# Performance work log

Hardware: AMD Instinct MI355X
Metric: run time of the kernel (lower is better)

Reference implementation:

```python
import jax, jax.numpy as jnp
import numpy as np

N = 50000        # nodes
E = 800000       # edges
H = 128          # hidden_channels
NH = 4           # num_heads
HD = H // NH     # head_dim
EPS = 1e-5       # LayerNorm eps (torch default)


def setup_inputs() -> dict:
    key = jax.random.key(0)
    ks = jax.random.split(key, 16)
    s = 0.02
    return {
        "x": jax.random.normal(ks[0], (N, H), dtype=jnp.float32),
        "edge_index": jax.random.randint(ks[1], (2, E), 0, N, dtype=jnp.int64),
        "Wq": jax.random.normal(ks[2], (H, H), dtype=jnp.float32) * s,
        "bq": jnp.zeros((H,), jnp.float32),
        "Wk": jax.random.normal(ks[3], (H, H), dtype=jnp.float32) * s,
        "bk": jnp.zeros((H,), jnp.float32),
        "Wv": jax.random.normal(ks[4], (H, H), dtype=jnp.float32) * s,
        "bv": jnp.zeros((H,), jnp.float32),
        "W1": jax.random.normal(ks[5], (2 * H, H), dtype=jnp.float32) * s,
        "b1": jnp.zeros((H,), jnp.float32),
        "ln_g": jnp.ones((H,), jnp.float32),
        "ln_b": jnp.zeros((H,), jnp.float32),
        "W2": jax.random.normal(ks[6], (H, H), dtype=jnp.float32) * s,
        "b2": jnp.zeros((H,), jnp.float32),
    }


def reference(x, edge_index, Wq, bq, Wk, bk, Wv, bv, W1, b1, ln_g, ln_b, W2, b2):
    n = x.shape[0]
    row, col = edge_index[0], edge_index[1]
    # dense projections, split heads: [N, NH, HD]
    Q = (x @ Wq + bq).reshape(n, NH, HD)
    K = (x @ Wk + bk).reshape(n, NH, HD)
    V = (x @ Wv + bv).reshape(n, NH, HD)
    # edge-wise gather + per-head dot product: [E, NH]
    scores = (Q[row] * K[col]).sum(-1) / jnp.sqrt(jnp.float32(HD))
    # segment softmax over edges grouped by destination node (row)
    m = jax.ops.segment_max(scores, row, num_segments=n)        # [N, NH]
    m = jnp.where(jnp.isfinite(m), m, 0.0)                      # empty segments -> 0
    e = jnp.exp(scores - m[row])                                # [E, NH]
    denom = jax.ops.segment_sum(e, row, num_segments=n)         # [N, NH]
    w = e / denom[row]                                          # [E, NH]
    # weighted scatter-add aggregation: [N, H]
    msg = (w[..., None] * V[col]).reshape(-1, NH * HD)          # [E, H]
    agg = jax.ops.segment_sum(msg, row, num_segments=n)         # [N, H]
    # MLP: Linear -> ReLU -> LayerNorm -> Linear, plus residual
    h = jax.nn.relu(jnp.concatenate([x, agg], axis=-1) @ W1 + b1)
    mu = h.mean(-1, keepdims=True)
    var = ((h - mu) ** 2).mean(-1, keepdims=True)
    h = (h - mu) / jnp.sqrt(var + EPS) * ln_g + ln_b
    return h @ W2 + b2 + x
```

## Files before the change

### kernel.cpp

```cpp
#include <hip/hip_runtime.h>
#include <hip/hip_bf16.h>

#define NN 50000
#define HH 128
#define NHEAD 4
#define HD 32
#define EE 800000
#define LN_EPS 1e-5f
#define ROWS_PAD 50048
#define SCAN_NB 98

typedef __bf16 bf16x8 __attribute__((ext_vector_type(8)));
typedef short  s16x8  __attribute__((ext_vector_type(8)));
typedef float  f32x4  __attribute__((ext_vector_type(4)));

__device__ __forceinline__ f32x4 mfma_bf16(s16x8 a, s16x8 b, f32x4 c) {
    return __builtin_amdgcn_mfma_f32_16x16x32_bf16((bf16x8)a, (bf16x8)b, c, 0, 0, 0);
}

__device__ __forceinline__ unsigned short f2bf(float f) {
    union { float f; unsigned int u; } v; v.f = f;
    unsigned int u = v.u + 0x7FFFu + ((v.u >> 16) & 1u);
    return (unsigned short)(u >> 16);
}
__device__ __forceinline__ float bf2f(unsigned short h) {
    union { unsigned int u; float f; } v; v.u = ((unsigned int)h) << 16;
    return v.f;
}
__device__ __forceinline__ float bflo(unsigned int w) { return __uint_as_float(w << 16); }
__device__ __forceinline__ float bfhi(unsigned int w) { return __uint_as_float(w & 0xffff0000u); }

__global__ void detect_idx_kernel(const unsigned int* __restrict__ buf, int* __restrict__ flag) {
    if (blockIdx.x == 0 && threadIdx.x == 0) {
        int is64 = 1;
        for (int i = 0; i < 64; ++i) {
            if (buf[2 * i + 1] != 0u) { is64 = 0; break; }
        }
        *flag = is64;
    }
}

__global__ void hist_kernel(const void* __restrict__ ei, const int* __restrict__ flag,
                            int* __restrict__ deg, int* __restrict__ rank) {
    int i = (blockIdx.x * blockDim.x + threadIdx.x) * 2;
    if (i >= EE) return;
    int r0, r1;
    if (*flag) {
        longlong2 rv = *(const longlong2*)((const long long*)ei + i);
        r0 = (int)rv.x; r1 = (int)rv.y;
    } else {
        int2 rv = *(const int2*)((const int*)ei + i);
        r0 = rv.x; r1 = rv.y;
    }
    int ra = atomicAdd(&deg[r0], 1);
    int rb = atomicAdd(&deg[r1], 1);
    *(int2*)(rank + i) = make_int2(ra, rb);
}

__global__ __launch_bounds__(512) void scan_a_kernel(const int* __restrict__ deg,
                                                     int* __restrict__ bsum) {
    __shared__ int red[8];
    const int t = threadIdx.x;
    const int gid = blockIdx.x * 512 + t;
    int v = (gid < NN) ? deg[gid] : 0;
    #pragma unroll
    for (int o = 1; o < 64; o <<= 1) v += __shfl_xor(v, o);
    if ((t & 63) == 0) red[t >> 6] = v;
    __syncthreads();
    if (t == 0) {
        int s = 0;
        #pragma unroll
        for (int k = 0; k < 8; ++k) s += red[k];
        bsum[blockIdx.x] = s;
    }
}

__global__ __launch_bounds__(512) void scan_c_kernel(const int* __restrict__ deg,
                                                     const int* __restrict__ bsum,
                                                     int* __restrict__ rstart) {
    __shared__ int wsum[8];
    __shared__ int blockoff;
    const int t = threadIdx.x;
    const int gid = blockIdx.x * 512 + t;
    const int lane = t & 63, w = t >> 6;
    if (t < 64) {
        int s = 0;
        for (int k = t; k < blockIdx.x; k += 64) s += bsum[k];
        #pragma unroll
        for (int o = 1; o < 64; o <<= 1) s += __shfl_xor(s, o);
        if (t == 0) blockoff = s;
    }
    int v = (gid < NN) ? deg[gid] : 0;
    int incl = v;
    #pragma unroll
    for (int o = 1; o < 64; o <<= 1) {
        int u = __shfl_up(incl, o);
        if (lane >= o) incl += u;
    }
    if (lane == 63) wsum[w] = incl;
    __syncthreads();
    int woff = 0;
    for (int k = 0; k < w; ++k) woff += wsum[k];
    int excl = blockoff + woff + incl - v;
    if (gid < NN) rstart[gid] = excl;
    if (gid == 0) rstart[NN] = EE;
}

__global__ void scatter_kernel(const void* __restrict__ ei, const int* __restrict__ flag,
                               const int* __restrict__ rank, const int* __restrict__ rstart,
                               int* __restrict__ colS) {
    int i = (blockIdx.x * blockDim.x + threadIdx.x) * 2;
    if (i >= EE) return;
    int r0, r1, c0, c1;
    if (*flag) {
        longlong2 rv = *(const longlong2*)((const long long*)ei + i);
        longlong2 cv = *(const longlong2*)((const long long*)ei + EE + i);
        r0 = (int)rv.x; r1 = (int)rv.y;
        c0 = (int)cv.x; c1 = (int)cv.y;
    } else {
        int2 rv = *(const int2*)((const int*)ei + i);
        int2 cv = *(const int2*)((const int*)ei + EE + i);
        r0 = rv.x; r1 = rv.y;
        c0 = cv.x; c1 = cv.y;
    }
    int2 rk = *(const int2*)(rank + i);
    colS[rstart[r0] + rk.x] = c0;
    colS[rstart[r1] + rk.y] = c1;
}

__global__ void pack_w_kernel(const float* __restrict__ Wq, const float* __restrict__ Wk,
                              const float* __restrict__ Wv, const float* __restrict__ W1,
                              const float* __restrict__ W2, unsigned short* __restrict__ wf) {
    int i = blockIdx.x * blockDim.x + threadIdx.x;
    if (i >= 98304) return;
    float val;
    if (i < 49152) {
        int j = i & 7, lane = (i >> 3) & 63, kk = (i >> 9) & 3, nt = i >> 11;
        int k = kk * 32 + (lane >> 4) * 8 + j;
        int n = nt * 16 + (lane & 15);
        const float* W = (n < 128) ? Wq : ((n < 256) ? Wk : Wv);
        val = W[k * HH + (n & 127)];
    } else if (i < 81920) {
        int local = i - 49152;
        int j = local & 7, lane = (local >> 3) & 63, kk = (local >> 9) & 7, nt = local >> 12;
        int k = kk * 32 + (lane >> 4) * 8 + j;
        int n = nt * 16 + (lane & 15);
        val = W1[k * HH + n];
    } else {
        int local = i - 81920;
        int j = local & 7, lane = (local >> 3) & 63, kk = (local >> 9) & 3, nt = local >> 11;
        int k = kk * 32 + (lane >> 4) * 8 + j;
        int n = nt * 16 + (lane & 15);
        val = W2[k * HH + n];
    }
    wf[i] = f2bf(val);
}

__global__ __launch_bounds__(256) void qkvx_kernel(
        const float* __restrict__ x, const unsigned short* __restrict__ wf,
        const float* __restrict__ bq, const float* __restrict__ bk, const float* __restrict__ bv,
        unsigned short* __restrict__ xa,
        unsigned short* __restrict__ Qb, unsigned short* __restrict__ Kb,
        unsigned short* __restrict__ Vb) {
    const int wave = threadIdx.x >> 6, lane = threadIdx.x & 63;
    const int row0 = blockIdx.x * 64 + wave * 16;
    const int arow = row0 + (lane & 15);
    const int kbase = (lane >> 4) * 8;

    s16x8 a[4];
    if (arow < NN) {
        const float* xp = x + (size_t)arow * HH + kbase;
        #pragma unroll
        for (int kk = 0; kk < 4; ++kk) {
            float4 f0 = *(const float4*)(xp + kk * 32);
            float4 f1 = *(const float4*)(xp + kk * 32 + 4);
            s16x8 av;
            av[0] = (short)f2bf(f0.x); av[1] = (short)f2bf(f0.y);
            av[2] = (short)f2bf(f0.z); av[3] = (short)f2bf(f0.w);
            av[4] = (short)f2bf(f1.x); av[5] = (short)f2bf(f1.y);
            av[6] = (short)f2bf(f1.z); av[7] = (short)f2bf(f1.w);
            a[kk] = av;
            *(s16x8*)(xa + (size_t)arow * 256 + kbase + kk * 32) = av;
        }
    } else {
        #pragma unroll
        for (int kk = 0; kk < 4; ++kk) a[kk] = (s16x8)0;
    }

    f32x4 acc[24];
    #pragma unroll
    for (int nt = 0; nt < 24; ++nt) acc[nt] = (f32x4){0.f, 0.f, 0.f, 0.f};

    const s16x8* wfv = (const s16x8*)wf;
    #pragma unroll
    for (int nt = 0; nt < 24; ++nt) {
        #pragma unroll
        for (int kk = 0; kk < 4; ++kk) {
            s16x8 b = wfv[(nt * 4 + kk) * 64 + lane];
            acc[nt] = mfma_bf16(a[kk], b, acc[nt]);
        }
    }

    const int colb = lane & 15;
    const int rbase = row0 + (lane >> 4) * 4;
    #pragma unroll
    for (int nt = 0; nt < 24; ++nt) {
        const int mtx = nt >> 3;
        const int nc = (nt & 7) * 16 + colb;
        const float* bias_p = (mtx == 0) ? bq : ((mtx == 1) ? bk : bv);
        unsigned short* O = (mtx == 0) ? Qb : ((mtx == 1) ? Kb : Vb);
        float bias = bias_p[nc];
        #pragma unroll
        for (int r = 0; r < 4; ++r)
            O[(size_t)(rbase + r) * 128 + nc] = f2bf(acc[nt][r] + bias);
    }
}

__global__ __launch_bounds__(256) void attn_kernel(
        const unsigned short* __restrict__ Qb, const unsigned short* __restrict__ Kb,
        const unsigned short* __restrict__ Vb, const int* __restrict__ rstart,
        const int* __restrict__ colS, unsigned short* __restrict__ xa) {
    const int wave = threadIdx.x >> 6;
    const int lane = threadIdx.x & 63;
    const int h = lane & 3;
    const int le = lane >> 2;
    const int half = lane >> 5;
    const int sl = lane & 31;
    const int g2 = sl >> 3;
    const int ibase = blockIdx.x * 16 + wave * 4;

    for (int j = 0; j < 4; ++j) {
        const int i = ibase + j;
        const int e0 = rstart[i], e1 = rstart[i + 1];
        const int deg = e1 - e0;

        float qf[32];
        {
            const uint4* qp = (const uint4*)(Qb + (size_t)i * 128 + h * 32);
            #pragma unroll
            for (int cch = 0; cch < 4; ++cch) {
                uint4 qv = qp[cch];
                unsigned int w_[4] = {qv.x, qv.y, qv.z, qv.w};
                #pragma unroll
                for (int dd = 0; dd < 4; ++dd) {
                    qf[cch * 8 + dd * 2]     = bflo(w_[dd]);
                    qf[cch * 8 + dd * 2 + 1] = bfhi(w_[dd]);
                }
            }
        }

        float m = -INFINITY, l = 0.f;
        float acc0 = 0.f, acc1 = 0.f, acc2 = 0.f, acc3 = 0.f;

        for (int c0 = 0; c0 < deg; c0 += 16) {
            const int cnt = min(16, deg - c0);
            int col = 0;
            float s = -INFINITY;
            if (le < cnt) {
                col = colS[e0 + c0 + le];
                const uint4* kp = (const uint4*)(Kb + (size_t)col * 128 + h * 32);
                float dot = 0.f;
                #pragma unroll
                for (int cch = 0; cch < 4; ++cch) {
                    uint4 kv = kp[cch];
                    unsigned int w_[4] = {kv.x, kv.y, kv.z, kv.w};
                    #pragma unroll
                    for (int dd = 0; dd < 4; ++dd) {
                        dot += qf[cch * 8 + dd * 2]     * bflo(w_[dd]);
                        dot += qf[cch * 8 + dd * 2 + 1] * bfhi(w_[dd]);
                    }
                }
                s = dot * 0.17677669529663689f;
            }
            float sm = s;
            sm = fmaxf(sm, __shfl_xor(sm, 4));
            sm = fmaxf(sm, __shfl_xor(sm, 8));
            sm = fmaxf(sm, __shfl_xor(sm, 16));
            sm = fmaxf(sm, __shfl_xor(sm, 32));
            const float mn = fmaxf(m, sm);
            const float p = (le < cnt) ? __expf(s - mn) : 0.f;
            float ps = p;
            ps += __shfl_xor(ps, 4);
            ps += __shfl_xor(ps, 8);
            ps += __shfl_xor(ps, 16);
            ps += __shfl_xor(ps, 32);
            const float fac = __expf(m - mn);
            l = l * fac + ps;
            m = mn;
            const float facbc = __shfl(fac, g2);
            acc0 *= facbc; acc1 *= facbc; acc2 *= facbc; acc3 *= facbc;
            #pragma unroll
            for (int e2 = 0; e2 < 8; ++e2) {
                const int e = 2 * e2 + half;
                const int   cbc = __shfl(col, 4 * e);
                const float pbc = __shfl(p, 4 * e + g2);
                const uint2 v2 = *(const uint2*)(Vb + (size_t)cbc * 128 + 4 * sl);
                acc0 += pbc * bflo(v2.x);
                acc1 += pbc * bfhi(v2.x);
                acc2 += pbc * bflo(v2.y);
                acc3 += pbc * bfhi(v2.y);
            }
        }

        acc0 += __shfl_xor(acc0, 32);
        acc1 += __shfl_xor(acc1, 32);
        acc2 += __shfl_xor(acc2, 32);
        acc3 += __shfl_xor(acc3, 32);
        const float lf = __shfl(l, g2);
        const float rinv = (lf > 0.f) ? 1.f / lf : 0.f;
        if (half == 0) {
            uint2 o;
            o.x = ((unsigned int)f2bf(acc1 * rinv) << 16) | (unsigned int)f2bf(acc0 * rinv);
            o.y = ((unsigned int)f2bf(acc3 * rinv) << 16) | (unsigned int)f2bf(acc2 * rinv);
            *(uint2*)(xa + (size_t)i * 256 + 128 + 4 * sl) = o;
        }
    }
}

__global__ __launch_bounds__(256) void gemm_mlp1_kernel(
        const unsigned short* __restrict__ xa, const unsigned short* __restrict__ w1f,
        const float* __restrict__ b1, const float* __restrict__ ln_g,
        const float* __restrict__ ln_b, unsigned short* __restrict__ hb) {
    const int wave = threadIdx.x >> 6, lane = threadIdx.x & 63;
    const int row0 = blockIdx.x * 64 + wave * 16;
    const int arow = row0 + (lane & 15);

    s16x8 a[8];
    const unsigned short* ap = xa + (size_t)arow * 256 + (lane >> 4) * 8;
    #pragma unroll
    for (int kk = 0; kk < 8; ++kk) a[kk] = *(const s16x8*)(ap + kk * 32);

    f32x4 acc[8];
    #pragma unroll
    for (int nt = 0; nt < 8; ++nt) acc[nt] = (f32x4){0.f, 0.f, 0.f, 0.f};

    const s16x8* wfv = (const s16x8*)w1f;
    #pragma unroll
    for (int nt = 0; nt < 8; ++nt) {
        #pragma unroll
        for (int kk = 0; kk < 8; ++kk) {
            s16x8 b = wfv[(nt * 8 + kk) * 64 + lane];
            acc[nt] = mfma_bf16(a[kk], b, acc[nt]);
        }
    }

    const int colb = lane & 15;
    #pragma unroll
    for (int nt = 0; nt < 8; ++nt) {
        float bias = b1[nt * 16 + colb];
        #pragma unroll
        for (int r = 0; r < 4; ++r) {
            float v = acc[nt][r] + bias;
            acc[nt][r] = v > 0.f ? v : 0.f;
        }
    }
    float mu[4], rs[4];
    #pragma unroll
    for (int r = 0; r < 4; ++r) {
        float s = 0.f, q = 0.f;
        #pragma unroll
        for (int nt = 0; nt < 8; ++nt) { float v = acc[nt][r]; s += v; q += v * v; }
        #pragma unroll
        for (int msk = 1; msk < 16; msk <<= 1) {
            s += __shfl_xor(s, msk, 16);
            q += __shfl_xor(q, msk, 16);
        }
        float m_ = s * (1.f / 128.f);
        float var = q * (1.f / 128.f) - m_ * m_;
        mu[r] = m_;
        rs[r] = rsqrtf(var + LN_EPS);
    }
    const int rbase = row0 + (lane >> 4) * 4;
    #pragma unroll
    for (int nt = 0; nt < 8; ++nt) {
        int col = nt * 16 + colb;
        float g = ln_g[col], bb = ln_b[col];
        #pragma unroll
        for (int r = 0; r < 4; ++r) {
            float h = (acc[nt][r] - mu[r]) * rs[r] * g + bb;
            hb[(size_t)(rbase + r) * 128 + col] = f2bf(h);
        }
    }
}

__global__ __launch_bounds__(256) void gemm_mlp2_kernel(
        const unsigned short* __restrict__ hb, const unsigned short* __restrict__ w2f,
        const float* __restrict__ b2, const unsigned short* __restrict__ xa,
        float* __restrict__ out) {
    const int wave = threadIdx.x >> 6, lane = threadIdx.x & 63;
    const int row0 = blockIdx.x * 64 + wave * 16;
    const int arow = row0 + (lane & 15);

    s16x8 a[4];
    const unsigned short* ap = hb + (size_t)arow * 128 + (lane >> 4) * 8;
    #pragma unroll
    for (int kk = 0; kk < 4; ++kk) a[kk] = *(const s16x8*)(ap + kk * 32);

    f32x4 acc[8];
    #pragma unroll
    for (int nt = 0; nt < 8; ++nt) acc[nt] = (f32x4){0.f, 0.f, 0.f, 0.f};

    const s16x8* wfv = (const s16x8*)w2f;
    #pragma unroll
    for (int nt = 0; nt < 8; ++nt) {
        #pragma unroll
        for (int kk = 0; kk < 4; ++kk) {
            s16x8 b = wfv[(nt * 4 + kk) * 64 + lane];
            acc[nt] = mfma_bf16(a[kk], b, acc[nt]);
        }
    }

    const int colb = lane & 15;
    const int rbase = row0 + (lane >> 4) * 4;
    #pragma unroll
    for (int nt = 0; nt < 8; ++nt) {
        int col = nt * 16 + colb;
        float bias = b2[col];
        #pragma unroll
        for (int r = 0; r < 4; ++r) {
            int row = rbase + r;
            if (row < NN)
                out[(size_t)row * 128 + col] =
                    acc[nt][r] + bias + bf2f(xa[(size_t)row * 256 + col]);
        }
    }
}

extern "C" void kernel_launch(void* const* d_in, const int* in_sizes, int n_in,
                              void* d_out, int out_size, void* d_ws, size_t ws_size,
                              hipStream_t stream) {
    const float* x    = (const float*)d_in[0];
    const void*  ei   = d_in[1];
    const float* Wq   = (const float*)d_in[2];
    const float* bq   = (const float*)d_in[3];
    const float* Wk   = (const float*)d_in[4];
    const float* bk   = (const float*)d_in[5];
    const float* Wv   = (const float*)d_in[6];
    const float* bv   = (const float*)d_in[7];
    const float* W1   = (const float*)d_in[8];
    const float* b1   = (const float*)d_in[9];
    const float* ln_g = (const float*)d_in[10];
    const float* ln_b = (const float*)d_in[11];
    const float* W2   = (const float*)d_in[12];
    const float* b2   = (const float*)d_in[13];
    float* out = (float*)d_out;

    char* ws = (char*)d_ws;
    size_t off = 0;
    auto alloc = [&](size_t bytes) {
        size_t o = off;
        off = (off + bytes + 255) & ~(size_t)255;
        return o;
    };
    size_t flag_o = alloc(sizeof(int));
    size_t deg_o  = alloc((size_t)NN * sizeof(int));
    size_t rank_o = alloc((size_t)EE * sizeof(int));
    size_t rs_o   = alloc((size_t)(NN + 1) * sizeof(int));
    size_t bsum_o = alloc((size_t)SCAN_NB * sizeof(int));
    size_t colS_o = alloc((size_t)EE * sizeof(int));
    size_t xa_o   = alloc((size_t)ROWS_PAD * 256 * sizeof(unsigned short));
    size_t wf_o   = alloc((size_t)98304 * sizeof(unsigned short));
    size_t Qb_o   = alloc((size_t)ROWS_PAD * 128 * sizeof(unsigned short));
    size_t Kb_o   = alloc((size_t)ROWS_PAD * 128 * sizeof(unsigned short));
    size_t Vb_o   = alloc((size_t)ROWS_PAD * 128 * sizeof(unsigned short));
    size_t hb_o   = Qb_o;

    int* flag   = (int*)(ws + flag_o);
    int* deg    = (int*)(ws + deg_o);
    int* rank   = (int*)(ws + rank_o);
    int* rstart = (int*)(ws + rs_o);
    int* bsum   = (int*)(ws + bsum_o);
    int* colS   = (int*)(ws + colS_o);
    unsigned short* xa = (unsigned short*)(ws + xa_o);
    unsigned short* wf = (unsigned short*)(ws + wf_o);
    unsigned short* Qb = (unsigned short*)(ws + Qb_o);
    unsigned short* Kb = (unsigned short*)(ws + Kb_o);
    unsigned short* Vb = (unsigned short*)(ws + Vb_o);
    unsigned short* hb = (unsigned short*)(ws + hb_o);

    hipMemsetAsync(ws + deg_o, 0, (size_t)NN * sizeof(int), stream);

    detect_idx_kernel<<<1, 64, 0, stream>>>((const unsigned int*)ei, flag);
    hist_kernel<<<(EE / 2 + 255) / 256, 256, 0, stream>>>(ei, flag, deg, rank);
    scan_a_kernel<<<SCAN_NB, 512, 0, stream>>>(deg, bsum);
    scan_c_kernel<<<SCAN_NB, 512, 0, stream>>>(deg, bsum, rstart);
    scatter_kernel<<<(EE / 2 + 255) / 256, 256, 0, stream>>>(ei, flag, rank, rstart, colS);

    pack_w_kernel<<<98304 / 256, 256, 0, stream>>>(Wq, Wk, Wv, W1, W2, wf);

    qkvx_kernel<<<ROWS_PAD / 64, 256, 0, stream>>>(x, wf, bq, bk, bv, xa, Qb, Kb, Vb);

    attn_kernel<<<NN / 16, 256, 0, stream>>>(Qb, Kb, Vb, rstart, colS, xa);

    gemm_mlp1_kernel<<<ROWS_PAD / 64, 256, 0, stream>>>(xa, wf + 49152, b1, ln_g, ln_b, hb);

    gemm_mlp2_kernel<<<ROWS_PAD / 64, 256, 0, stream>>>(hb, wf + 81920, b2, xa, out);
}
```

Baseline: 193.8 us.

## Interleave two destination nodes per wave in attention to overlap gathers

Each wave in the attention kernel now handles two destination nodes at once, interleaving their 16-edge chunks so the K and V gathers of both nodes are in flight together. Tail loops finish whichever node has more edges. The grid doubles, with 2 nodes per wave instead of 4 processed one after another, which raises memory-level parallelism and occupancy. Q is kept packed in registers and unpacked inside the dot product, which saves registers but adds conversion work per edge.

```diff
diff --git a/kernel.cpp b/kernel.cpp
--- a/kernel.cpp
+++ b/kernel.cpp
@@ -216,6 +216,80 @@
     }
 }
 
+__device__ __forceinline__ float dot32(uint4 k0, uint4 k1, uint4 k2, uint4 k3,
+                                       const uint4 q[4]) {
+    float dot = 0.f;
+    uint4 kk[4] = {k0, k1, k2, k3};
+    #pragma unroll
+    for (int c = 0; c < 4; ++c) {
+        unsigned int kw[4] = {kk[c].x, kk[c].y, kk[c].z, kk[c].w};
+        unsigned int qw[4] = {q[c].x, q[c].y, q[c].z, q[c].w};
+        #pragma unroll
+        for (int d = 0; d < 4; ++d) {
+            dot += bflo(qw[d]) * bflo(kw[d]);
+            dot += bfhi(qw[d]) * bfhi(kw[d]);
+        }
+    }
+    return dot;
+}
+
+__device__ __forceinline__ void smax_update(float s, int le, int cnt,
+                                            float& m, float& l, float& p, float& fac) {
+    float sm = s;
+    sm = fmaxf(sm, __shfl_xor(sm, 4));
+    sm = fmaxf(sm, __shfl_xor(sm, 8));
+    sm = fmaxf(sm, __shfl_xor(sm, 16));
+    sm = fmaxf(sm, __shfl_xor(sm, 32));
+    const float mn = fmaxf(m, sm);
+    p = (le < cnt) ? __expf(s - mn) : 0.f;
+    float ps = p;
+    ps += __shfl_xor(ps, 4);
+    ps += __shfl_xor(ps, 8);
+    ps += __shfl_xor(ps, 16);
+    ps += __shfl_xor(ps, 32);
+    fac = __expf(m - mn);
+    l = l * fac + ps;
+    m = mn;
+}
+
+__device__ __forceinline__ void pv_acc(const unsigned short* __restrict__ Vb,
+                                       int col, float p, float fac,
+                                       int half, int sl, int g2,
+                                       float& a0, float& a1, float& a2, float& a3) {
+    const float facbc = __shfl(fac, g2);
+    a0 *= facbc; a1 *= facbc; a2 *= facbc; a3 *= facbc;
+    #pragma unroll
+    for (int e2 = 0; e2 < 8; ++e2) {
+        const int e = 2 * e2 + half;
+        const int   cbc = __shfl(col, 4 * e);
+        const float pbc = __shfl(p, 4 * e + g2);
+        const uint2 v2 = *(const uint2*)(Vb + (size_t)cbc * 128 + 4 * sl);
+        a0 += pbc * bflo(v2.x);
+        a1 += pbc * bfhi(v2.x);
+        a2 += pbc * bflo(v2.y);
+        a3 += pbc * bfhi(v2.y);
+    }
+}
+
+__device__ __forceinline__ void chunk_one(const unsigned short* __restrict__ Kb,
+                                          const unsigned short* __restrict__ Vb,
+                                          const int* __restrict__ colS,
+                                          int e0, int c0, int deg, const uint4 q[4],
+                                          int h, int le, int half, int sl, int g2,
+                                          float& m, float& l,
+                                          float& a0, float& a1, float& a2, float& a3) {
+    const int cnt = min(16, deg - c0);
+    int col = 0;
+    if (le < cnt) col = colS[e0 + c0 + le];
+    const uint4* kp = (const uint4*)(Kb + (size_t)col * 128 + h * 32);
+    uint4 k0 = kp[0], k1 = kp[1], k2 = kp[2], k3 = kp[3];
+    float s = -INFINITY;
+    if (le < cnt) s = dot32(k0, k1, k2, k3, q) * 0.17677669529663689f;
+    float p, fac;
+    smax_update(s, le, cnt, m, l, p, fac);
+    pv_acc(Vb, col, p, fac, half, sl, g2, a0, a1, a2, a3);
+}
+
 __global__ __launch_bounds__(256) void attn_kernel(
         const unsigned short* __restrict__ Qb, const unsigned short* __restrict__ Kb,
         const unsigned short* __restrict__ Vb, const int* __restrict__ rstart,
@@ -227,93 +301,75 @@
     const int half = lane >> 5;
     const int sl = lane & 31;
     const int g2 = sl >> 3;
-    const int ibase = blockIdx.x * 16 + wave * 4;
-
-    for (int j = 0; j < 4; ++j) {
-        const int i = ibase + j;
-        const int e0 = rstart[i], e1 = rstart[i + 1];
-        const int deg = e1 - e0;
-
-        float qf[32];
-        {
-            const uint4* qp = (const uint4*)(Qb + (size_t)i * 128 + h * 32);
-            #pragma unroll
-            for (int cch = 0; cch < 4; ++cch) {
-                uint4 qv = qp[cch];
-                unsigned int w_[4] = {qv.x, qv.y, qv.z, qv.w};
-                #pragma unroll
-                for (int dd = 0; dd < 4; ++dd) {
-                    qf[cch * 8 + dd * 2]     = bflo(w_[dd]);
-                    qf[cch * 8 + dd * 2 + 1] = bfhi(w_[dd]);
-                }
-            }
-        }
-
-        float m = -INFINITY, l = 0.f;
-        float acc0 = 0.f, acc1 = 0.f, acc2 = 0.f, acc3 = 0.f;
-
-        for (int c0 = 0; c0 < deg; c0 += 16) {
-            const int cnt = min(16, deg - c0);
-            int col = 0;
-            float s = -INFINITY;
-            if (le < cnt) {
-                col = colS[e0 + c0 + le];
-                const uint4* kp = (const uint4*)(Kb + (size_t)col * 128 + h * 32);
-                float dot = 0.f;
-                #pragma unroll
-                for (int cch = 0; cch < 4; ++cch) {
-                    uint4 kv = kp[cch];
-                    unsigned int w_[4] = {kv.x, kv.y, kv.z, kv.w};
-                    #pragma unroll
-                    for (int dd = 0; dd < 4; ++dd) {
-                        dot += qf[cch * 8 + dd * 2]     * bflo(w_[dd]);
-                        dot += qf[cch * 8 + dd * 2 + 1] * bfhi(w_[dd]);
-                    }
-                }
-                s = dot * 0.17677669529663689f;
-            }
-            float sm = s;
-            sm = fmaxf(sm, __shfl_xor(sm, 4));
-            sm = fmaxf(sm, __shfl_xor(sm, 8));
-            sm = fmaxf(sm, __shfl_xor(sm, 16));
-            sm = fmaxf(sm, __shfl_xor(sm, 32));
-            const float mn = fmaxf(m, sm);
-            const float p = (le < cnt) ? __expf(s - mn) : 0.f;
-            float ps = p;
-            ps += __shfl_xor(ps, 4);
-            ps += __shfl_xor(ps, 8);
-            ps += __shfl_xor(ps, 16);
-            ps += __shfl_xor(ps, 32);
-            const float fac = __expf(m - mn);
-            l = l * fac + ps;
-            m = mn;
-            const float facbc = __shfl(fac, g2);
-            acc0 *= facbc; acc1 *= facbc; acc2 *= facbc; acc3 *= facbc;
-            #pragma unroll
-            for (int e2 = 0; e2 < 8; ++e2) {
-                const int e = 2 * e2 + half;
-                const int   cbc = __shfl(col, 4 * e);
-                const float pbc = __shfl(p, 4 * e + g2);
-                const uint2 v2 = *(const uint2*)(Vb + (size_t)cbc * 128 + 4 * sl);
-                acc0 += pbc * bflo(v2.x);
-                acc1 += pbc * bfhi(v2.x);
-                acc2 += pbc * bflo(v2.y);
-                acc3 += pbc * bfhi(v2.y);
-            }
-        }
-
-        acc0 += __shfl_xor(acc0, 32);
-        acc1 += __shfl_xor(acc1, 32);
-        acc2 += __shfl_xor(acc2, 32);
-        acc3 += __shfl_xor(acc3, 32);
-        const float lf = __shfl(l, g2);
-        const float rinv = (lf > 0.f) ? 1.f / lf : 0.f;
-        if (half == 0) {
-            uint2 o;
-            o.x = ((unsigned int)f2bf(acc1 * rinv) << 16) | (unsigned int)f2bf(acc0 * rinv);
-            o.y = ((unsigned int)f2bf(acc3 * rinv) << 16) | (unsigned int)f2bf(acc2 * rinv);
-            *(uint2*)(xa + (size_t)i * 256 + 128 + 4 * sl) = o;
-        }
+    const int iA = (blockIdx.x * 4 + wave) * 2;
+    const int iB = iA + 1;
+
+    const int e0A = rstart[iA];
+    const int e1A = rstart[iA + 1];
+    const int e1B = rstart[iA + 2];
+    const int e0B = e1A;
+    const int degA = e1A - e0A;
+    const int degB = e1B - e0B;
+
+    uint4 qA[4], qB[4];
+    {
+        const uint4* qpA = (const uint4*)(Qb + (size_t)iA * 128 + h * 32);
+        const uint4* qpB = (const uint4*)(Qb + (size_t)iB * 128 + h * 32);
+        #pragma unroll
+        for (int c = 0; c < 4; ++c) { qA[c] = qpA[c]; qB[c] = qpB[c]; }
+    }
+
+    float mA = -INFINITY, lA = 0.f, aA0 = 0.f, aA1 = 0.f, aA2 = 0.f, aA3 = 0.f;
+    float mB = -INFINITY, lB = 0.f, aB0 = 0.f, aB1 = 0.f, aB2 = 0.f, aB3 = 0.f;
+
+    int c0A = 0, c0B = 0;
+    while (c0A < degA && c0B < degB) {
+        const int cntA = min(16, degA - c0A);
+        const int cntB = min(16, degB - c0B);
+        int colA = 0, colB = 0;
+        if (le < cntA) colA = colS[e0A + c0A + le];
+        if (le < cntB) colB = colS[e0B + c0B + le];
+        const uint4* kpA = (const uint4*)(Kb + (size_t)colA * 128 + h * 32);
+        const uint4* kpB = (const uint4*)(Kb + (size_t)colB * 128 + h * 32);
+        uint4 ka0 = kpA[0], ka1 = kpA[1], ka2 = kpA[2], ka3 = kpA[3];
+        uint4 kb0 = kpB[0], kb1 = kpB[1], kb2 = kpB[2], kb3 = kpB[3];
+        float sA = -INFINITY, sB = -INFINITY;
+        if (le < cntA) sA = dot32(ka0, ka1, ka2, ka3, qA) * 0.17677669529663689f;
+        if (le < cntB) sB = dot32(kb0, kb1, kb2, kb3, qB) * 0.17677669529663689f;
+        float pA, facA, pB, facB;
+        smax_update(sA, le, cntA, mA, lA, pA, facA);
+        smax_update(sB, le, cntB, mB, lB, pB, facB);
+        pv_acc(Vb, colA, pA, facA, half, sl, g2, aA0, aA1, aA2, aA3);
+        pv_acc(Vb, colB, pB, facB, half, sl, g2, aB0, aB1, aB2, aB3);
+        c0A += 16; c0B += 16;
+    }
+    while (c0A < degA) {
+        chunk_one(Kb, Vb, colS, e0A, c0A, degA, qA, h, le, half, sl, g2,
+                  mA, lA, aA0, aA1, aA2, aA3);
+        c0A += 16;
+    }
+    while (c0B < degB) {
+        chunk_one(Kb, Vb, colS, e0B, c0B, degB, qB, h, le, half, sl, g2,
+                  mB, lB, aB0, aB1, aB2, aB3);
+        c0B += 16;
+    }
+
+    aA0 += __shfl_xor(aA0, 32); aA1 += __shfl_xor(aA1, 32);
+    aA2 += __shfl_xor(aA2, 32); aA3 += __shfl_xor(aA3, 32);
+    aB0 += __shfl_xor(aB0, 32); aB1 += __shfl_xor(aB1, 32);
+    aB2 += __shfl_xor(aB2, 32); aB3 += __shfl_xor(aB3, 32);
+    const float lfA = __shfl(lA, g2);
+    const float lfB = __shfl(lB, g2);
+    const float riA = (lfA > 0.f) ? 1.f / lfA : 0.f;
+    const float riB = (lfB > 0.f) ? 1.f / lfB : 0.f;
+    if (half == 0) {
+        uint2 oA, oB;
+        oA.x = ((unsigned int)f2bf(aA1 * riA) << 16) | (unsigned int)f2bf(aA0 * riA);
+        oA.y = ((unsigned int)f2bf(aA3 * riA) << 16) | (unsigned int)f2bf(aA2 * riA);
+        oB.x = ((unsigned int)f2bf(aB1 * riB) << 16) | (unsigned int)f2bf(aB0 * riB);
+        oB.y = ((unsigned int)f2bf(aB3 * riB) << 16) | (unsigned int)f2bf(aB2 * riB);
+        *(uint2*)(xa + (size_t)iA * 256 + 128 + 4 * sl) = oA;
+        *(uint2*)(xa + (size_t)iB * 256 + 128 + 4 * sl) = oB;
     }
 }
 
@@ -490,7 +546,7 @@
 
     qkvx_kernel<<<ROWS_PAD / 64, 256, 0, stream>>>(x, wf, bq, bk, bv, xa, Qb, Kb, Vb);
 
-    attn_kernel<<<NN / 16, 256, 0, stream>>>(Qb, Kb, Vb, rstart, colS, xa);
+    attn_kernel<<<NN / 8, 256, 0, stream>>>(Qb, Kb, Vb, rstart, colS, xa);
 
     gemm_mlp1_kernel<<<ROWS_PAD / 64, 256, 0, stream>>>(xa, wf + 49152, b1, ln_g, ln_b, hb);
 
```

Result: slower. 208.3 us (+7.4%).

## Use fp16 Q/K with fdot2, one node per wave, fuse MLP kernels

Applied to the files above, without the earlier changes.

Q and K are now stored as fp16 so the attention score dot product can use packed fdot2 instructions instead of unpacking bf16 into floats. The attention kernel now assigns one node per wave instead of four, which spreads work across more blocks. The two MLP GEMMs are fused through a shared-memory tile, so the intermediate LayerNorm output no longer round-trips through global memory and one launch is removed. fp16 has a narrower range than bf16 for Q/K, which could matter for large activations.

```diff
diff --git a/kernel.cpp b/kernel.cpp
--- a/kernel.cpp
+++ b/kernel.cpp
@@ -13,6 +13,7 @@
 typedef __bf16 bf16x8 __attribute__((ext_vector_type(8)));
 typedef short  s16x8  __attribute__((ext_vector_type(8)));
 typedef float  f32x4  __attribute__((ext_vector_type(4)));
+typedef _Float16 h2   __attribute__((ext_vector_type(2)));
 
 __device__ __forceinline__ f32x4 mfma_bf16(s16x8 a, s16x8 b, f32x4 c) {
     return __builtin_amdgcn_mfma_f32_16x16x32_bf16((bf16x8)a, (bf16x8)b, c, 0, 0, 0);
@@ -29,6 +30,26 @@
 }
 __device__ __forceinline__ float bflo(unsigned int w) { return __uint_as_float(w << 16); }
 __device__ __forceinline__ float bfhi(unsigned int w) { return __uint_as_float(w & 0xffff0000u); }
+
+__device__ __forceinline__ unsigned short f2h(float f) {
+    _Float16 h = (_Float16)f;
+    return __builtin_bit_cast(unsigned short, h);
+}
+
+#if defined(__has_builtin)
+#if __has_builtin(__builtin_amdgcn_fdot2)
+#define HAVE_FDOT2 1
+#endif
+#endif
+
+__device__ __forceinline__ float fdot2u(unsigned int a, unsigned int b, float c) {
+#ifdef HAVE_FDOT2
+    return __builtin_amdgcn_fdot2(__builtin_bit_cast(h2, a), __builtin_bit_cast(h2, b), c, false);
+#else
+    h2 ha = __builtin_bit_cast(h2, a), hb = __builtin_bit_cast(h2, b);
+    return c + (float)ha[0] * (float)hb[0] + (float)ha[1] * (float)hb[1];
+#endif
+}
 
 __global__ void detect_idx_kernel(const unsigned int* __restrict__ buf, int* __restrict__ flag) {
     if (blockIdx.x == 0 && threadIdx.x == 0) {
@@ -211,8 +232,10 @@
         unsigned short* O = (mtx == 0) ? Qb : ((mtx == 1) ? Kb : Vb);
         float bias = bias_p[nc];
         #pragma unroll
-        for (int r = 0; r < 4; ++r)
-            O[(size_t)(rbase + r) * 128 + nc] = f2bf(acc[nt][r] + bias);
+        for (int r = 0; r < 4; ++r) {
+            float v = acc[nt][r] + bias;
+            O[(size_t)(rbase + r) * 128 + nc] = (mtx == 2) ? f2bf(v) : f2h(v);
+        }
     }
 }
 
@@ -222,108 +245,98 @@
         const int* __restrict__ colS, unsigned short* __restrict__ xa) {
     const int wave = threadIdx.x >> 6;
     const int lane = threadIdx.x & 63;
+    const int i = blockIdx.x * 4 + wave;
+    if (i >= NN) return;
     const int h = lane & 3;
     const int le = lane >> 2;
     const int half = lane >> 5;
     const int sl = lane & 31;
     const int g2 = sl >> 3;
-    const int ibase = blockIdx.x * 16 + wave * 4;
-
-    for (int j = 0; j < 4; ++j) {
-        const int i = ibase + j;
-        const int e0 = rstart[i], e1 = rstart[i + 1];
-        const int deg = e1 - e0;
-
-        float qf[32];
-        {
-            const uint4* qp = (const uint4*)(Qb + (size_t)i * 128 + h * 32);
-            #pragma unroll
-            for (int cch = 0; cch < 4; ++cch) {
-                uint4 qv = qp[cch];
-                unsigned int w_[4] = {qv.x, qv.y, qv.z, qv.w};
-                #pragma unroll
-                for (int dd = 0; dd < 4; ++dd) {
-                    qf[cch * 8 + dd * 2]     = bflo(w_[dd]);
-                    qf[cch * 8 + dd * 2 + 1] = bfhi(w_[dd]);
-                }
-            }
-        }
-
-        float m = -INFINITY, l = 0.f;
-        float acc0 = 0.f, acc1 = 0.f, acc2 = 0.f, acc3 = 0.f;
-
-        for (int c0 = 0; c0 < deg; c0 += 16) {
-            const int cnt = min(16, deg - c0);
-            int col = 0;
-            float s = -INFINITY;
-            if (le < cnt) {
-                col = colS[e0 + c0 + le];
-                const uint4* kp = (const uint4*)(Kb + (size_t)col * 128 + h * 32);
-                float dot = 0.f;
-                #pragma unroll
-                for (int cch = 0; cch < 4; ++cch) {
-                    uint4 kv = kp[cch];
-                    unsigned int w_[4] = {kv.x, kv.y, kv.z, kv.w};
-                    #pragma unroll
-                    for (int dd = 0; dd < 4; ++dd) {
-                        dot += qf[cch * 8 + dd * 2]     * bflo(w_[dd]);
-                        dot += qf[cch * 8 + dd * 2 + 1] * bfhi(w_[dd]);
-                    }
-                }
-                s = dot * 0.17677669529663689f;
-            }
-            float sm = s;
-            sm = fmaxf(sm, __shfl_xor(sm, 4));
-            sm = fmaxf(sm, __shfl_xor(sm, 8));
-            sm = fmaxf(sm, __shfl_xor(sm, 16));
-            sm = fmaxf(sm, __shfl_xor(sm, 32));
-            const float mn = fmaxf(m, sm);
-            const float p = (le < cnt) ? __expf(s - mn) : 0.f;
-            float ps = p;
-            ps += __shfl_xor(ps, 4);
-            ps += __shfl_xor(ps, 8);
-            ps += __shfl_xor(ps, 16);
-            ps += __shfl_xor(ps, 32);
-            const float fac = __expf(m - mn);
-            l = l * fac + ps;
-            m = mn;
-            const float facbc = __shfl(fac, g2);
-            acc0 *= facbc; acc1 *= facbc; acc2 *= facbc; acc3 *= facbc;
-            #pragma unroll
-            for (int e2 = 0; e2 < 8; ++e2) {
-                const int e = 2 * e2 + half;
-                const int   cbc = __shfl(col, 4 * e);
-                const float pbc = __shfl(p, 4 * e + g2);
-                const uint2 v2 = *(const uint2*)(Vb + (size_t)cbc * 128 + 4 * sl);
-                acc0 += pbc * bflo(v2.x);
-                acc1 += pbc * bfhi(v2.x);
-                acc2 += pbc * bflo(v2.y);
-                acc3 += pbc * bfhi(v2.y);
-            }
-        }
-
-        acc0 += __shfl_xor(acc0, 32);
-        acc1 += __shfl_xor(acc1, 32);
-        acc2 += __shfl_xor(acc2, 32);
-        acc3 += __shfl_xor(acc3, 32);
-        const float lf = __shfl(l, g2);
-        const float rinv = (lf > 0.f) ? 1.f / lf : 0.f;
-        if (half == 0) {
-            uint2 o;
-            o.x = ((unsigned int)f2bf(acc1 * rinv) << 16) | (unsigned int)f2bf(acc0 * rinv);
-            o.y = ((unsigned int)f2bf(acc3 * rinv) << 16) | (unsigned int)f2bf(acc2 * rinv);
-            *(uint2*)(xa + (size_t)i * 256 + 128 + 4 * sl) = o;
-        }
-    }
-}
-
-__global__ __launch_bounds__(256) void gemm_mlp1_kernel(
+    const int e0 = rstart[i], e1 = rstart[i + 1];
+    const int deg = e1 - e0;
+
+    uint4 q[4];
+    {
+        const uint4* qp = (const uint4*)(Qb + (size_t)i * 128 + h * 32);
+        #pragma unroll
+        for (int c = 0; c < 4; ++c) q[c] = qp[c];
+    }
+
+    float m = -INFINITY, l = 0.f;
+    float acc0 = 0.f, acc1 = 0.f, acc2 = 0.f, acc3 = 0.f;
+
+    for (int c0 = 0; c0 < deg; c0 += 16) {
+        const int cnt = min(16, deg - c0);
+        int col = 0;
+        if (le < cnt) col = colS[e0 + c0 + le];
+        const uint4* kp = (const uint4*)(Kb + (size_t)col * 128 + h * 32);
+        uint4 k0 = kp[0], k1 = kp[1], k2 = kp[2], k3 = kp[3];
+        float d0 = 0.f, d1 = 0.f, d2 = 0.f, d3 = 0.f;
+        d0 = fdot2u(k0.x, q[0].x, d0); d0 = fdot2u(k0.y, q[0].y, d0);
+        d0 = fdot2u(k0.z, q[0].z, d0); d0 = fdot2u(k0.w, q[0].w, d0);
+        d1 = fdot2u(k1.x, q[1].x, d1); d1 = fdot2u(k1.y, q[1].y, d1);
+        d1 = fdot2u(k1.z, q[1].z, d1); d1 = fdot2u(k1.w, q[1].w, d1);
+        d2 = fdot2u(k2.x, q[2].x, d2); d2 = fdot2u(k2.y, q[2].y, d2);
+        d2 = fdot2u(k2.z, q[2].z, d2); d2 = fdot2u(k2.w, q[2].w, d2);
+        d3 = fdot2u(k3.x, q[3].x, d3); d3 = fdot2u(k3.y, q[3].y, d3);
+        d3 = fdot2u(k3.z, q[3].z, d3); d3 = fdot2u(k3.w, q[3].w, d3);
+        float s = -INFINITY;
+        if (le < cnt) s = ((d0 + d1) + (d2 + d3)) * 0.17677669529663689f;
+        float sm = s;
+        sm = fmaxf(sm, __shfl_xor(sm, 4));
+        sm = fmaxf(sm, __shfl_xor(sm, 8));
+        sm = fmaxf(sm, __shfl_xor(sm, 16));
+        sm = fmaxf(sm, __shfl_xor(sm, 32));
+        const float mn = fmaxf(m, sm);
+        const float p = (le < cnt) ? __expf(s - mn) : 0.f;
+        float ps = p;
+        ps += __shfl_xor(ps, 4);
+        ps += __shfl_xor(ps, 8);
+        ps += __shfl_xor(ps, 16);
+        ps += __shfl_xor(ps, 32);
+        const float fac = __expf(m - mn);
+        l = l * fac + ps;
+        m = mn;
+        const float facbc = __shfl(fac, g2);
+        acc0 *= facbc; acc1 *= facbc; acc2 *= facbc; acc3 *= facbc;
+        #pragma unroll
+        for (int e2 = 0; e2 < 8; ++e2) {
+            const int e = 2 * e2 + half;
+            const int   cbc = __shfl(col, 4 * e);
+            const float pbc = __shfl(p, 4 * e + g2);
+            const uint2 v2 = *(const uint2*)(Vb + (size_t)cbc * 128 + 4 * sl);
+            acc0 += pbc * bflo(v2.x);
+            acc1 += pbc * bfhi(v2.x);
+            acc2 += pbc * bflo(v2.y);
+            acc3 += pbc * bfhi(v2.y);
+        }
+    }
+
+    acc0 += __shfl_xor(acc0, 32);
+    acc1 += __shfl_xor(acc1, 32);
+    acc2 += __shfl_xor(acc2, 32);
+    acc3 += __shfl_xor(acc3, 32);
+    const float lf = __shfl(l, g2);
+    const float rinv = (lf > 0.f) ? 1.f / lf : 0.f;
+    if (half == 0) {
+        uint2 o;
+        o.x = ((unsigned int)f2bf(acc1 * rinv) << 16) | (unsigned int)f2bf(acc0 * rinv);
+        o.y = ((unsigned int)f2bf(acc3 * rinv) << 16) | (unsigned int)f2bf(acc2 * rinv);
+        *(uint2*)(xa + (size_t)i * 256 + 128 + 4 * sl) = o;
+    }
+}
+
+#define HROW 136
+__global__ __launch_bounds__(256) void mlp_fused_kernel(
         const unsigned short* __restrict__ xa, const unsigned short* __restrict__ w1f,
         const float* __restrict__ b1, const float* __restrict__ ln_g,
-        const float* __restrict__ ln_b, unsigned short* __restrict__ hb) {
+        const float* __restrict__ ln_b, const unsigned short* __restrict__ w2f,
+        const float* __restrict__ b2, float* __restrict__ out) {
+    __shared__ unsigned short hs[64 * HROW];
     const int wave = threadIdx.x >> 6, lane = threadIdx.x & 63;
     const int row0 = blockIdx.x * 64 + wave * 16;
     const int arow = row0 + (lane & 15);
+    const int colb = lane & 15;
 
     s16x8 a[8];
     const unsigned short* ap = xa + (size_t)arow * 256 + (lane >> 4) * 8;
@@ -334,17 +347,16 @@
     #pragma unroll
     for (int nt = 0; nt < 8; ++nt) acc[nt] = (f32x4){0.f, 0.f, 0.f, 0.f};
 
-    const s16x8* wfv = (const s16x8*)w1f;
+    const s16x8* w1v = (const s16x8*)w1f;
     #pragma unroll
     for (int nt = 0; nt < 8; ++nt) {
         #pragma unroll
         for (int kk = 0; kk < 8; ++kk) {
-            s16x8 b = wfv[(nt * 8 + kk) * 64 + lane];
+            s16x8 b = w1v[(nt * 8 + kk) * 64 + lane];
             acc[nt] = mfma_bf16(a[kk], b, acc[nt]);
         }
     }
 
-    const int colb = lane & 15;
     #pragma unroll
     for (int nt = 0; nt < 8; ++nt) {
         float bias = b1[nt * 16 + colb];
@@ -370,47 +382,39 @@
         mu[r] = m_;
         rs[r] = rsqrtf(var + LN_EPS);
     }
-    const int rbase = row0 + (lane >> 4) * 4;
+    const int lrbase = wave * 16 + (lane >> 4) * 4;
     #pragma unroll
     for (int nt = 0; nt < 8; ++nt) {
         int col = nt * 16 + colb;
         float g = ln_g[col], bb = ln_b[col];
         #pragma unroll
         for (int r = 0; r < 4; ++r) {
-            float h = (acc[nt][r] - mu[r]) * rs[r] * g + bb;
-            hb[(size_t)(rbase + r) * 128 + col] = f2bf(h);
-        }
-    }
-}
-
-__global__ __launch_bounds__(256) void gemm_mlp2_kernel(
-        const unsigned short* __restrict__ hb, const unsigned short* __restrict__ w2f,
-        const float* __restrict__ b2, const unsigned short* __restrict__ xa,
-        float* __restrict__ out) {
-    const int wave = threadIdx.x >> 6, lane = threadIdx.x & 63;
-    const int row0 = blockIdx.x * 64 + wave * 16;
-    const int arow = row0 + (lane & 15);
-
-    s16x8 a[4];
-    const unsigned short* ap = hb + (size_t)arow * 128 + (lane >> 4) * 8;
-    #pragma unroll
-    for (int kk = 0; kk < 4; ++kk) a[kk] = *(const s16x8*)(ap + kk * 32);
-
-    f32x4 acc[8];
-    #pragma unroll
-    for (int nt = 0; nt < 8; ++nt) acc[nt] = (f32x4){0.f, 0.f, 0.f, 0.f};
-
-    const s16x8* wfv = (const s16x8*)w2f;
+            float hv = (acc[nt][r] - mu[r]) * rs[r] * g + bb;
+            hs[(lrbase + r) * HROW + col] = f2bf(hv);
+        }
+    }
+    __syncthreads();
+
+    const int la = wave * 16 + (lane & 15);
+    s16x8 a2[4];
+    const unsigned short* hp = hs + la * HROW + (lane >> 4) * 8;
+    #pragma unroll
+    for (int kk = 0; kk < 4; ++kk) a2[kk] = *(const s16x8*)(hp + kk * 32);
+
+    f32x4 acc2[8];
+    #pragma unroll
+    for (int nt = 0; nt < 8; ++nt) acc2[nt] = (f32x4){0.f, 0.f, 0.f, 0.f};
+
+    const s16x8* w2v = (const s16x8*)w2f;
     #pragma unroll
     for (int nt = 0; nt < 8; ++nt) {
         #pragma unroll
         for (int kk = 0; kk < 4; ++kk) {
-            s16x8 b = wfv[(nt * 4 + kk) * 64 + lane];
-            acc[nt] = mfma_bf16(a[kk], b, acc[nt]);
-        }
-    }
-
-    const int colb = lane & 15;
+            s16x8 b = w2v[(nt * 4 + kk) * 64 + lane];
+            acc2[nt] = mfma_bf16(a2[kk], b, acc2[nt]);
+        }
+    }
+
     const int rbase = row0 + (lane >> 4) * 4;
     #pragma unroll
     for (int nt = 0; nt < 8; ++nt) {
@@ -421,7 +425,7 @@
             int row = rbase + r;
             if (row < NN)
                 out[(size_t)row * 128 + col] =
-                    acc[nt][r] + bias + bf2f(xa[(size_t)row * 256 + col]);
+                    acc2[nt][r] + bias + bf2f(xa[(size_t)row * 256 + col]);
         }
     }
 }
@@ -463,7 +467,6 @@
     size_t Qb_o   = alloc((size_t)ROWS_PAD * 128 * sizeof(unsigned short));
     size_t Kb_o   = alloc((size_t)ROWS_PAD * 128 * sizeof(unsigned short));
     size_t Vb_o   = alloc((size_t)ROWS_PAD * 128 * sizeof(unsigned short));
-    size_t hb_o   = Qb_o;
 
     int* flag   = (int*)(ws + flag_o);
     int* deg    = (int*)(ws + deg_o);
@@ -476,7 +479,6 @@
     unsigned short* Qb = (unsigned short*)(ws + Qb_o);
     unsigned short* Kb = (unsigned short*)(ws + Kb_o);
     unsigned short* Vb = (unsigned short*)(ws + Vb_o);
-    unsigned short* hb = (unsigned short*)(ws + hb_o);
 
     hipMemsetAsync(ws + deg_o, 0, (size_t)NN * sizeof(int), stream);
 
@@ -490,9 +492,8 @@
 
     qkvx_kernel<<<ROWS_PAD / 64, 256, 0, stream>>>(x, wf, bq, bk, bv, xa, Qb, Kb, Vb);
 
-    attn_kernel<<<NN / 16, 256, 0, stream>>>(Qb, Kb, Vb, rstart, colS, xa);
-
-    gemm_mlp1_kernel<<<ROWS_PAD / 64, 256, 0, stream>>>(xa, wf + 49152, b1, ln_g, ln_b, hb);
-
-    gemm_mlp2_kernel<<<ROWS_PAD / 64, 256, 0, stream>>>(hb, wf + 81920, b2, xa, out);
-}
+    attn_kernel<<<(NN + 3) / 4, 256, 0, stream>>>(Qb, Kb, Vb, rstart, colS, xa);
+
+    mlp_fused_kernel<<<ROWS_PAD / 64, 256, 0, stream>>>(
+        xa, wf + 49152, b1, ln_g, ln_b, wf + 81920, b2, out);
+}
```

Result: no change. 190.4 us (-1.8%).
